# Optimization experiments

Measured on AMD Instinct MI355X. Metric: run time of the kernel, lower is better.

Reference implementation:

```python
import jax, jax.numpy as jnp
import numpy as np

N = 50000          # nodes
E = 400000         # random edges (self-loops added in reference, per PyG default)
IN, HID, HEADS, OUT = 20, 64, 4, 256
NEG_SLOPE = 0.2    # GATv2Conv default negative_slope
EPS = 1e-16        # PyG softmax denom epsilon


def setup_inputs() -> dict:
    key = jax.random.key(0)
    ks = jax.random.split(key, 14)
    g = lambda k, shape, scale=0.1: (jax.random.normal(k, shape, jnp.float32) * scale)
    return {
        "x": jax.random.normal(ks[0], (N, IN), jnp.float32),
        "edge_index": jax.random.randint(ks[1], (2, E), 0, N, jnp.int32),
        # layer 1: GATv2Conv(IN -> HID, heads=HEADS, concat=True)
        "W_l1": g(ks[2], (IN, HEADS * HID)),
        "b_l1": jnp.zeros((HEADS * HID,), jnp.float32),
        "W_r1": g(ks[3], (IN, HEADS * HID)),
        "b_r1": jnp.zeros((HEADS * HID,), jnp.float32),
        "att1": g(ks[4], (HEADS, HID)),
        "bias1": jnp.zeros((HEADS * HID,), jnp.float32),
        # layer 2: GATv2Conv(HEADS*HID -> OUT, heads=1, concat=False)
        "W_l2": g(ks[5], (HEADS * HID, OUT)),
        "b_l2": jnp.zeros((OUT,), jnp.float32),
        "W_r2": g(ks[6], (HEADS * HID, OUT)),
        "b_r2": jnp.zeros((OUT,), jnp.float32),
        "att2": g(ks[7], (1, OUT)),
        "bias2": jnp.zeros((OUT,), jnp.float32),
    }


def _gatv2_layer(x, src, dst, W_l, b_l, W_r, b_r, att, bias, heads, ch, concat):
    n = x.shape[0]
    x_l = (x @ W_l + b_l).reshape(n, heads, ch)  # source transform
    x_r = (x @ W_r + b_r).reshape(n, heads, ch)  # target transform
    # GATv2: e_ij = att . LeakyReLU(x_l[j] + x_r[i])   (j->i edge)
    pre = jax.nn.leaky_relu(x_l[src] + x_r[dst], NEG_SLOPE)       # [E, H, C]
    logits = jnp.einsum('ehc,hc->eh', pre, att)                    # [E, H]
    # segment softmax over destination node (self-loops guarantee nonempty)
    m = jax.ops.segment_max(logits, dst, num_segments=n)
    w = jnp.exp(logits - m[dst])
    denom = jax.ops.segment_sum(w, dst, num_segments=n)
    alpha = w / (denom[dst] + EPS)                                 # [E, H]
    out = jax.ops.segment_sum(x_l[src] * alpha[:, :, None], dst, num_segments=n)
    out = out.reshape(n, heads * ch) if concat else out.mean(axis=1)
    return out + bias


def reference(x, edge_index, W_l1, b_l1, W_r1, b_r1, att1, bias1,
              W_l2, b_l2, W_r2, b_r2, att2, bias2):
    n = x.shape[0]
    loop = jnp.arange(n, dtype=edge_index.dtype)  # PyG add_self_loops=True
    src = jnp.concatenate([edge_index[0], loop])
    dst = jnp.concatenate([edge_index[1], loop])
    h = _gatv2_layer(x, src, dst, W_l1, b_l1, W_r1, b_r1, att1, bias1, HEADS, HID, True)
    h = jax.nn.elu(h)
    out = _gatv2_layer(h, src, dst, W_l2, b_l2, W_r2, b_r2, att2, bias2, 1, OUT, False)
    return out
```

## Files before the change

kernel.cpp:

```cpp
#include <hip/hip_runtime.h>
#include <hip/hip_bf16.h>
#include <math.h>

#define CH 256
#define SCAN_BLOCK 1024

typedef short bf16x8 __attribute__((ext_vector_type(8)));
typedef float f32x4 __attribute__((ext_vector_type(4)));

__device__ __forceinline__ float lrelu(float v) { return fmaxf(v, 0.2f * v); }
__device__ __forceinline__ float elu(float v)   { return v > 0.f ? v : __expf(v) - 1.f; }

__device__ __forceinline__ unsigned short f2bf(float f) {
    unsigned u = __float_as_uint(f);
    return (unsigned short)((u + 0x7fffu + ((u >> 16) & 1u)) >> 16);
}
__device__ __forceinline__ float4 ldbf4(const unsigned short* rowbase, int lane) {
    uint2 u = ((const uint2*)rowbase)[lane];
    return make_float4(__uint_as_float(u.x << 16), __uint_as_float(u.x & 0xffff0000u),
                       __uint_as_float(u.y << 16), __uint_as_float(u.y & 0xffff0000u));
}
__device__ __forceinline__ void stbf4(unsigned short* rowbase, int lane, float4 v) {
    uint2 u;
    u.x = (unsigned)f2bf(v.x) | ((unsigned)f2bf(v.y) << 16);
    u.y = (unsigned)f2bf(v.z) | ((unsigned)f2bf(v.w) << 16);
    ((uint2*)rowbase)[lane] = u;
}

__global__ __launch_bounds__(256) void gemm1_kernel(const float* __restrict__ x,
                             const float* __restrict__ Wl, const float* __restrict__ bl,
                             const float* __restrict__ Wr, const float* __restrict__ br,
                             unsigned short* __restrict__ xl, unsigned short* __restrict__ xr, int n) {
    __shared__ float xs[64][20];
    int n0 = blockIdx.x * 64;
    int tid = threadIdx.x;
    for (int i = tid; i < 64 * 20; i += 256) {
        int m = i / 20, k = i % 20;
        int row = n0 + m;
        xs[m][k] = (row < n) ? x[(size_t)row * 20 + k] : 0.f;
    }
    int c = tid;
    float wl[20], wr[20];
#pragma unroll
    for (int k = 0; k < 20; ++k) { wl[k] = Wl[k * 256 + c]; wr[k] = Wr[k * 256 + c]; }
    float blv = bl[c], brv = br[c];
    __syncthreads();
#pragma unroll 1
    for (int g = 0; g < 8; ++g) {
        int base = g * 8;
        float al[8], ar[8];
#pragma unroll
        for (int m = 0; m < 8; ++m) { al[m] = blv; ar[m] = brv; }
#pragma unroll
        for (int k = 0; k < 20; ++k) {
            float wlv = wl[k], wrv = wr[k];
#pragma unroll
            for (int m = 0; m < 8; ++m) {
                float xv = xs[base + m][k];
                al[m] += xv * wlv;
                ar[m] += xv * wrv;
            }
        }
#pragma unroll
        for (int m = 0; m < 8; ++m) {
            int row = n0 + base + m;
            if (row < n) {
                xl[(size_t)row * 256 + c] = f2bf(al[m]);
                xr[(size_t)row * 256 + c] = f2bf(ar[m]);
            }
        }
    }
}

__global__ void count_deg(const int* __restrict__ ei, int* __restrict__ deg, int e) {
    int t = blockIdx.x * blockDim.x + threadIdx.x;
    if (t < e) atomicAdd(&deg[ei[e + t]], 1);
}

__global__ void scan_block_k(const int* __restrict__ deg, int* __restrict__ rowptr,
                             int* __restrict__ bsums, int n) {
    __shared__ int wsum[16];
    __shared__ int woff[17];
    int tid = threadIdx.x;
    int gi = blockIdx.x * SCAN_BLOCK + tid;
    int lane = tid & 63, wid = tid >> 6;
    int v = (gi < n) ? deg[gi] : 0;
    int incl = v;
#pragma unroll
    for (int d = 1; d < 64; d <<= 1) {
        int t = __shfl_up(incl, d, 64);
        if (lane >= d) incl += t;
    }
    if (lane == 63) wsum[wid] = incl;
    __syncthreads();
    if (tid < 16) {
        int s = wsum[tid];
#pragma unroll
        for (int d = 1; d < 16; d <<= 1) {
            int t = __shfl_up(s, d, 64);
            if (tid >= d) s += t;
        }
        woff[tid + 1] = s;
        if (tid == 0) woff[0] = 0;
    }
    __syncthreads();
    incl += woff[wid];
    if (gi < n) rowptr[gi + 1] = incl;
    if (tid == 0) bsums[blockIdx.x] = woff[16];
}

__global__ void scan_tops_k(int* bsums, int nb) {
    int tid = threadIdx.x;
    int v = (tid < nb) ? bsums[tid] : 0;
    int incl = v;
#pragma unroll
    for (int d = 1; d < 64; d <<= 1) {
        int t = __shfl_up(incl, d, 64);
        if (tid >= d) incl += t;
    }
    if (tid < nb) bsums[tid] = incl - v;
}

__global__ void scan_fix_k(int* __restrict__ rowptr, int* __restrict__ cursor,
                           const int* __restrict__ deg, const int* __restrict__ bsums, int n) {
    int gi = blockIdx.x * SCAN_BLOCK + threadIdx.x;
    if (gi >= n) return;
    int off = bsums[blockIdx.x];
    int incl = rowptr[gi + 1] + off;
    rowptr[gi + 1] = incl;
    cursor[gi] = incl - deg[gi];
    if (gi == 0) rowptr[0] = 0;
}

__global__ void scatter_k(const int* __restrict__ ei, int* __restrict__ cursor,
                          int* __restrict__ csr, int e) {
    int t = blockIdx.x * blockDim.x + threadIdx.x;
    if (t >= e) return;
    int s = ei[t], d = ei[e + t];
    int idx = atomicAdd(&cursor[d], 1);
    csr[idx] = s;
}

__global__ void fused_gat1(const unsigned short* __restrict__ xl, const unsigned short* __restrict__ xr,
                           const int* __restrict__ rowptr, const int* __restrict__ csr,
                           const float* __restrict__ att, const float* __restrict__ bias,
                           unsigned short* __restrict__ hout, int n) {
    int wid = threadIdx.x >> 6;
    int lane = threadIdx.x & 63;
    int i = blockIdx.x * 4 + wid;
    if (i >= n) return;
    float4 xr4 = ldbf4(xr + (size_t)i * CH, lane);
    float4 a4  = ((const float4*)att)[lane];
    float4 xli = ldbf4(xl + (size_t)i * CH, lane);
    float ps = lrelu(xli.x + xr4.x) * a4.x + lrelu(xli.y + xr4.y) * a4.y +
               lrelu(xli.z + xr4.z) * a4.z + lrelu(xli.w + xr4.w) * a4.w;
    ps += __shfl_xor(ps, 1); ps += __shfl_xor(ps, 2);
    ps += __shfl_xor(ps, 4); ps += __shfl_xor(ps, 8);
    float m = ps, l = 1.f;
    float4 acc = xli;
    int beg = rowptr[i], end = rowptr[i + 1];
    for (int e = beg; e < end; e += 8) {
        int cnt = end - e;
        int ss[8];
#pragma unroll
        for (int j = 0; j < 8; ++j) ss[j] = (j < cnt) ? csr[e + j] : i;
        float4 rr[8];
#pragma unroll
        for (int j = 0; j < 8; ++j) rr[j] = ldbf4(xl + (size_t)ss[j] * CH, lane);
        float pp[8];
#pragma unroll
        for (int j = 0; j < 8; ++j)
            pp[j] = lrelu(rr[j].x + xr4.x) * a4.x + lrelu(rr[j].y + xr4.y) * a4.y +
                    lrelu(rr[j].z + xr4.z) * a4.z + lrelu(rr[j].w + xr4.w) * a4.w;
#pragma unroll
        for (int d = 1; d < 16; d <<= 1)
#pragma unroll
            for (int j = 0; j < 8; ++j) pp[j] += __shfl_xor(pp[j], d);
#pragma unroll
        for (int j = 0; j < 8; ++j) if (j >= cnt) pp[j] = -INFINITY;
        float mx = m;
#pragma unroll
        for (int j = 0; j < 8; ++j) mx = fmaxf(mx, pp[j]);
        float sc = __expf(m - mx);
        float ww[8];
#pragma unroll
        for (int j = 0; j < 8; ++j) ww[j] = __expf(pp[j] - mx);
        l *= sc;
        acc.x *= sc; acc.y *= sc; acc.z *= sc; acc.w *= sc;
#pragma unroll
        for (int j = 0; j < 8; ++j) {
            l += ww[j];
            acc.x += ww[j] * rr[j].x;
            acc.y += ww[j] * rr[j].y;
            acc.z += ww[j] * rr[j].z;
            acc.w += ww[j] * rr[j].w;
        }
        m = mx;
    }
    float inv = 1.f / (l + 1e-16f);
    float4 b4 = ((const float4*)bias)[lane];
    float4 o;
    o.x = elu(acc.x * inv + b4.x);
    o.y = elu(acc.y * inv + b4.y);
    o.z = elu(acc.z * inv + b4.z);
    o.w = elu(acc.w * inv + b4.w);
    stbf4(hout + (size_t)i * CH, lane, o);
}

__global__ void fused_gat2(const unsigned short* __restrict__ xl, const unsigned short* __restrict__ xr,
                           const int* __restrict__ rowptr, const int* __restrict__ csr,
                           const float* __restrict__ att, const float* __restrict__ bias,
                           float* __restrict__ out, int n) {
    int wid = threadIdx.x >> 6;
    int lane = threadIdx.x & 63;
    int i = blockIdx.x * 4 + wid;
    if (i >= n) return;
    float4 xr4 = ldbf4(xr + (size_t)i * CH, lane);
    float4 a4  = ((const float4*)att)[lane];
    float4 xli = ldbf4(xl + (size_t)i * CH, lane);
    float ps = lrelu(xli.x + xr4.x) * a4.x + lrelu(xli.y + xr4.y) * a4.y +
               lrelu(xli.z + xr4.z) * a4.z + lrelu(xli.w + xr4.w) * a4.w;
    ps += __shfl_xor(ps, 1); ps += __shfl_xor(ps, 2); ps += __shfl_xor(ps, 4);
    ps += __shfl_xor(ps, 8); ps += __shfl_xor(ps, 16); ps += __shfl_xor(ps, 32);
    float m = ps, l = 1.f;
    float4 acc = xli;
    int beg = rowptr[i], end = rowptr[i + 1];
    for (int e = beg; e < end; e += 8) {
        int cnt = end - e;
        int ss[8];
#pragma unroll
        for (int j = 0; j < 8; ++j) ss[j] = (j < cnt) ? csr[e + j] : i;
        float4 rr[8];
#pragma unroll
        for (int j = 0; j < 8; ++j) rr[j] = ldbf4(xl + (size_t)ss[j] * CH, lane);
        float pp[8];
#pragma unroll
        for (int j = 0; j < 8; ++j)
            pp[j] = lrelu(rr[j].x + xr4.x) * a4.x + lrelu(rr[j].y + xr4.y) * a4.y +
                    lrelu(rr[j].z + xr4.z) * a4.z + lrelu(rr[j].w + xr4.w) * a4.w;
#pragma unroll
        for (int d = 1; d < 64; d <<= 1)
#pragma unroll
            for (int j = 0; j < 8; ++j) pp[j] += __shfl_xor(pp[j], d);
#pragma unroll
        for (int j = 0; j < 8; ++j) if (j >= cnt) pp[j] = -INFINITY;
        float mx = m;
#pragma unroll
        for (int j = 0; j < 8; ++j) mx = fmaxf(mx, pp[j]);
        float sc = __expf(m - mx);
        float ww[8];
#pragma unroll
        for (int j = 0; j < 8; ++j) ww[j] = __expf(pp[j] - mx);
        l *= sc;
        acc.x *= sc; acc.y *= sc; acc.z *= sc; acc.w *= sc;
#pragma unroll
        for (int j = 0; j < 8; ++j) {
            l += ww[j];
            acc.x += ww[j] * rr[j].x;
            acc.y += ww[j] * rr[j].y;
            acc.z += ww[j] * rr[j].z;
            acc.w += ww[j] * rr[j].w;
        }
        m = mx;
    }
    float inv = 1.f / (l + 1e-16f);
    float4 b4 = ((const float4*)bias)[lane];
    float4 o;
    o.x = acc.x * inv + b4.x;
    o.y = acc.y * inv + b4.y;
    o.z = acc.z * inv + b4.z;
    o.w = acc.w * inv + b4.w;
    ((float4*)(out + (size_t)i * CH))[lane] = o;
}

__global__ void wconv(const float* __restrict__ Wl2, const float* __restrict__ Wr2,
                      unsigned short* __restrict__ Wt) {
    int t = blockIdx.x * 256 + threadIdx.x;
    int z = t >> 16;
    int idx = t & 65535;
    int k = idx >> 8, nn = idx & 255;
    const float* W = z ? Wr2 : Wl2;
    Wt[z * 65536 + nn * 256 + k] = f2bf(W[k * 256 + nn]);
}

#define LDA2 264
#define LDC2 136
__global__ __launch_bounds__(256) void gemm_mfma(
        const unsigned short* __restrict__ A,
        const unsigned short* __restrict__ Wt,
        const float* __restrict__ ba, const float* __restrict__ bb,
        unsigned short* __restrict__ Ca, unsigned short* __restrict__ Cb, int M) {
    int b = blockIdx.x;
    int y = b & 1, mt = b >> 1;
    int m0 = mt * 64, n0 = y * 128;

    __shared__ unsigned short As[64 * LDA2];
    __shared__ unsigned short Cs[64 * LDC2];

    int tid = threadIdx.x, lane = tid & 63, wn = tid >> 6;
    int q = lane >> 4, l15 = lane & 15;

    {
        int row = tid >> 2, quarter = tid & 3;
        bool ok = (m0 + row) < M;
        const uint4* gA = (const uint4*)(A + (size_t)(m0 + row) * 256 + quarter * 64);
        uint4* sA = (uint4*)(As + row * LDA2 + quarter * 64);
        const uint4 z4 = make_uint4(0, 0, 0, 0);
        uint4 v[8];
#pragma unroll
        for (int i = 0; i < 8; ++i) v[i] = ok ? gA[i] : z4;
#pragma unroll
        for (int i = 0; i < 8; ++i) sA[i] = v[i];
    }
    __syncthreads();

    const unsigned short* gB = Wt + (size_t)(n0 + wn * 32 + l15) * 256 + q * 8;

    bf16x8 b_cur[2], b_nxt[2];
#pragma unroll
    for (int j = 0; j < 2; ++j) {
        b_cur[j] = *(const bf16x8*)(gB + j * 16 * 256);
        b_nxt[j] = b_cur[j];
    }

#pragma unroll
    for (int z = 0; z < 2; ++z) {
        f32x4 acc[4][2];
#pragma unroll
        for (int i = 0; i < 4; ++i)
#pragma unroll
            for (int j = 0; j < 2; ++j) acc[i][j] = (f32x4){0.f, 0.f, 0.f, 0.f};

#pragma unroll
        for (int kb = 0; kb < 8; ++kb) {
            if (!(z == 1 && kb == 7)) {
                int zn = (kb == 7) ? 1 : z;
                int kn = (kb == 7) ? 0 : kb + 1;
#pragma unroll
                for (int j = 0; j < 2; ++j)
                    b_nxt[j] = *(const bf16x8*)(gB + (size_t)zn * 65536 + j * 16 * 256 + kn * 32);
            }
            bf16x8 a[4];
#pragma unroll
            for (int i = 0; i < 4; ++i)
                a[i] = *(const bf16x8*)&As[(i * 16 + l15) * LDA2 + kb * 32 + q * 8];
#pragma unroll
            for (int i = 0; i < 4; ++i)
#pragma unroll
                for (int j = 0; j < 2; ++j)
                    acc[i][j] = __builtin_amdgcn_mfma_f32_16x16x32_bf16(a[i], b_cur[j], acc[i][j], 0, 0, 0);
#pragma unroll
            for (int j = 0; j < 2; ++j) b_cur[j] = b_nxt[j];
        }

        const float* bias = z ? bb : ba;
        unsigned short* C = z ? Cb : Ca;
#pragma unroll
        for (int j = 0; j < 2; ++j) {
            int col = wn * 32 + j * 16 + l15;
            float bcol = bias[n0 + col];
#pragma unroll
            for (int i = 0; i < 4; ++i) {
#pragma unroll
                for (int rr = 0; rr < 4; ++rr)
                    Cs[(i * 16 + q * 4 + rr) * LDC2 + col] = f2bf(acc[i][j][rr] + bcol);
            }
        }
        __syncthreads();
        {
            int row = tid >> 2, seg = tid & 3;
            if (m0 + row < M) {
                const uint4* src = (const uint4*)&Cs[row * LDC2 + seg * 32];
                uint4* dst = (uint4*)(C + (size_t)(m0 + row) * 256 + n0 + seg * 32);
#pragma unroll
                for (int i = 0; i < 4; ++i) dst[i] = src[i];
            }
        }
        __syncthreads();
    }
}

extern "C" void kernel_launch(void* const* d_in, const int* in_sizes, int n_in,
                              void* d_out, int out_size, void* d_ws, size_t ws_size,
                              hipStream_t stream) {
    const float* x    = (const float*)d_in[0];
    const int*   ei   = (const int*)d_in[1];
    const float* Wl1  = (const float*)d_in[2];
    const float* bl1  = (const float*)d_in[3];
    const float* Wr1  = (const float*)d_in[4];
    const float* br1  = (const float*)d_in[5];
    const float* att1 = (const float*)d_in[6];
    const float* bias1= (const float*)d_in[7];
    const float* Wl2  = (const float*)d_in[8];
    const float* bl2  = (const float*)d_in[9];
    const float* Wr2  = (const float*)d_in[10];
    const float* br2  = (const float*)d_in[11];
    const float* att2 = (const float*)d_in[12];
    const float* bias2= (const float*)d_in[13];

    int n = in_sizes[0] / 20;
    int e = in_sizes[1] / 2;
    float* out = (float*)d_out;
    size_t nch = (size_t)n * CH;

    unsigned short* buf0 = (unsigned short*)d_ws;
    unsigned short* buf1 = buf0 + nch;
    unsigned short* hbuf = buf1 + nch;
    unsigned short* wt2  = hbuf + nch;
    int* deg    = (int*)(wt2 + 2 * 65536);
    int* rowptr = deg + n;
    int* cursor = rowptr + n + 1;
    int* bsums  = cursor + n;
    int* csr    = bsums + 64;

    hipMemsetAsync(deg, 0, (size_t)n * sizeof(int), stream);

    gemm1_kernel<<<(n + 63) / 64, 256, 0, stream>>>(x, Wl1, bl1, Wr1, br1, buf0, buf1, n);

    count_deg<<<(e + 255) / 256, 256, 0, stream>>>(ei, deg, e);
    int nb = (n + SCAN_BLOCK - 1) / SCAN_BLOCK;
    scan_block_k<<<nb, SCAN_BLOCK, 0, stream>>>(deg, rowptr, bsums, n);
    scan_tops_k<<<1, 64, 0, stream>>>(bsums, nb);
    scan_fix_k<<<nb, SCAN_BLOCK, 0, stream>>>(rowptr, cursor, deg, bsums, n);
    scatter_k<<<(e + 255) / 256, 256, 0, stream>>>(ei, cursor, csr, e);

    wconv<<<512, 256, 0, stream>>>(Wl2, Wr2, wt2);

    fused_gat1<<<(n + 3) / 4, 256, 0, stream>>>(buf0, buf1, rowptr, csr, att1, bias1, hbuf, n);

    gemm_mfma<<<((n + 63) / 64) * 2, 256, 0, stream>>>(hbuf, wt2, bl2, br2, buf0, buf1, n);

    fused_gat2<<<(n + 3) / 4, 256, 0, stream>>>(buf0, buf1, rowptr, csr, att2, bias2, out, n);
}
```

Measured before the change: 340.5 us.

## Prefetch next neighbor batch and drop online max in GAT softmax

Both fused GAT aggregation kernels now load the next batch of 8 neighbor feature rows into registers while the current batch is being processed. They also replace the online-softmax running max and rescaling with direct exponentials of the logits. The aim is to hide gather latency and cut the per-batch max, rescale and extra exp work. In exchange it raises register pressure, and it risks overflow or precision loss if attention logits become large.

```diff
diff --git a/kernel.cpp b/kernel.cpp
--- a/kernel.cpp
+++ b/kernel.cpp
@@ -15,10 +15,12 @@
     unsigned u = __float_as_uint(f);
     return (unsigned short)((u + 0x7fffu + ((u >> 16) & 1u)) >> 16);
 }
-__device__ __forceinline__ float4 ldbf4(const unsigned short* rowbase, int lane) {
-    uint2 u = ((const uint2*)rowbase)[lane];
+__device__ __forceinline__ float4 bf4(uint2 u) {
     return make_float4(__uint_as_float(u.x << 16), __uint_as_float(u.x & 0xffff0000u),
                        __uint_as_float(u.y << 16), __uint_as_float(u.y & 0xffff0000u));
+}
+__device__ __forceinline__ float4 ldbf4(const unsigned short* rowbase, int lane) {
+    return bf4(((const uint2*)rowbase)[lane]);
 }
 __device__ __forceinline__ void stbf4(unsigned short* rowbase, int lane, float4 v) {
     uint2 u;
@@ -156,17 +158,31 @@
                lrelu(xli.z + xr4.z) * a4.z + lrelu(xli.w + xr4.w) * a4.w;
     ps += __shfl_xor(ps, 1); ps += __shfl_xor(ps, 2);
     ps += __shfl_xor(ps, 4); ps += __shfl_xor(ps, 8);
-    float m = ps, l = 1.f;
-    float4 acc = xli;
+    float ws = __expf(ps);
+    float l = ws;
+    float4 acc = make_float4(ws * xli.x, ws * xli.y, ws * xli.z, ws * xli.w);
     int beg = rowptr[i], end = rowptr[i + 1];
+
+    uint2 raw[8];
+#pragma unroll
+    for (int j = 0; j < 8; ++j) {
+        int s = (beg + j < end) ? csr[beg + j] : i;
+        raw[j] = ((const uint2*)(xl + (size_t)s * CH))[lane];
+    }
     for (int e = beg; e < end; e += 8) {
-        int cnt = end - e;
-        int ss[8];
-#pragma unroll
-        for (int j = 0; j < 8; ++j) ss[j] = (j < cnt) ? csr[e + j] : i;
+        int rem = end - e;
+        bool more = (e + 8) < end;
+        uint2 raw2[8];
+        if (more) {
+#pragma unroll
+            for (int j = 0; j < 8; ++j) {
+                int s = (e + 8 + j < end) ? csr[e + 8 + j] : i;
+                raw2[j] = ((const uint2*)(xl + (size_t)s * CH))[lane];
+            }
+        }
         float4 rr[8];
 #pragma unroll
-        for (int j = 0; j < 8; ++j) rr[j] = ldbf4(xl + (size_t)ss[j] * CH, lane);
+        for (int j = 0; j < 8; ++j) rr[j] = bf4(raw[j]);
         float pp[8];
 #pragma unroll
         for (int j = 0; j < 8; ++j)
@@ -176,17 +192,9 @@
         for (int d = 1; d < 16; d <<= 1)
 #pragma unroll
             for (int j = 0; j < 8; ++j) pp[j] += __shfl_xor(pp[j], d);
-#pragma unroll
-        for (int j = 0; j < 8; ++j) if (j >= cnt) pp[j] = -INFINITY;
-        float mx = m;
-#pragma unroll
-        for (int j = 0; j < 8; ++j) mx = fmaxf(mx, pp[j]);
-        float sc = __expf(m - mx);
         float ww[8];
 #pragma unroll
-        for (int j = 0; j < 8; ++j) ww[j] = __expf(pp[j] - mx);
-        l *= sc;
-        acc.x *= sc; acc.y *= sc; acc.z *= sc; acc.w *= sc;
+        for (int j = 0; j < 8; ++j) ww[j] = (j < rem) ? __expf(pp[j]) : 0.f;
 #pragma unroll
         for (int j = 0; j < 8; ++j) {
             l += ww[j];
@@ -195,7 +203,10 @@
             acc.z += ww[j] * rr[j].z;
             acc.w += ww[j] * rr[j].w;
         }
-        m = mx;
+        if (more) {
+#pragma unroll
+            for (int j = 0; j < 8; ++j) raw[j] = raw2[j];
+        }
     }
     float inv = 1.f / (l + 1e-16f);
     float4 b4 = ((const float4*)bias)[lane];
@@ -222,17 +233,31 @@
                lrelu(xli.z + xr4.z) * a4.z + lrelu(xli.w + xr4.w) * a4.w;
     ps += __shfl_xor(ps, 1); ps += __shfl_xor(ps, 2); ps += __shfl_xor(ps, 4);
     ps += __shfl_xor(ps, 8); ps += __shfl_xor(ps, 16); ps += __shfl_xor(ps, 32);
-    float m = ps, l = 1.f;
-    float4 acc = xli;
+    float ws = __expf(ps);
+    float l = ws;
+    float4 acc = make_float4(ws * xli.x, ws * xli.y, ws * xli.z, ws * xli.w);
     int beg = rowptr[i], end = rowptr[i + 1];
+
+    uint2 raw[8];
+#pragma unroll
+    for (int j = 0; j < 8; ++j) {
+        int s = (beg + j < end) ? csr[beg + j] : i;
+        raw[j] = ((const uint2*)(xl + (size_t)s * CH))[lane];
+    }
     for (int e = beg; e < end; e += 8) {
-        int cnt = end - e;
-        int ss[8];
-#pragma unroll
-        for (int j = 0; j < 8; ++j) ss[j] = (j < cnt) ? csr[e + j] : i;
+        int rem = end - e;
+        bool more = (e + 8) < end;
+        uint2 raw2[8];
+        if (more) {
+#pragma unroll
+            for (int j = 0; j < 8; ++j) {
+                int s = (e + 8 + j < end) ? csr[e + 8 + j] : i;
+                raw2[j] = ((const uint2*)(xl + (size_t)s * CH))[lane];
+            }
+        }
         float4 rr[8];
 #pragma unroll
-        for (int j = 0; j < 8; ++j) rr[j] = ldbf4(xl + (size_t)ss[j] * CH, lane);
+        for (int j = 0; j < 8; ++j) rr[j] = bf4(raw[j]);
         float pp[8];
 #pragma unroll
         for (int j = 0; j < 8; ++j)
@@ -242,17 +267,9 @@
         for (int d = 1; d < 64; d <<= 1)
 #pragma unroll
             for (int j = 0; j < 8; ++j) pp[j] += __shfl_xor(pp[j], d);
-#pragma unroll
-        for (int j = 0; j < 8; ++j) if (j >= cnt) pp[j] = -INFINITY;
-        float mx = m;
-#pragma unroll
-        for (int j = 0; j < 8; ++j) mx = fmaxf(mx, pp[j]);
-        float sc = __expf(m - mx);
         float ww[8];
 #pragma unroll
-        for (int j = 0; j < 8; ++j) ww[j] = __expf(pp[j] - mx);
-        l *= sc;
-        acc.x *= sc; acc.y *= sc; acc.z *= sc; acc.w *= sc;
+        for (int j = 0; j < 8; ++j) ww[j] = (j < rem) ? __expf(pp[j]) : 0.f;
 #pragma unroll
         for (int j = 0; j < 8; ++j) {
             l += ww[j];
@@ -261,7 +278,10 @@
             acc.z += ww[j] * rr[j].z;
             acc.w += ww[j] * rr[j].w;
         }
-        m = mx;
+        if (more) {
+#pragma unroll
+            for (int j = 0; j < 8; ++j) raw[j] = raw2[j];
+        }
     }
     float inv = 1.f / (l + 1e-16f);
     float4 b4 = ((const float4*)bias)[lane];
```

Result: slower. 387.1 us (+13.7%).
